# Kernel optimization log

Measured on AMD Instinct MI355X. Metric: run time of the kernel, lower is better.

Reference implementation:

```python
import jax, jax.numpy as jnp
import numpy as np
from math import sqrt

T, B, V = 32, 16, 30000
D, DQKV = 300, 150
K, G = 10, 32            # top-K globals, grapharea_size neighbours each
S = 25000                # last_idx_senses (= SC rows)
EPS = 1e-8


def setup_inputs() -> dict:
    key = jax.random.key(0)
    ks = jax.random.split(key, 6)
    return {
        "predictions_globals": jax.random.normal(ks[0], (T, B, V), jnp.float32),
        "location_context": jax.random.normal(ks[1], (T, B, D), jnp.float32),
        "SC": jax.random.normal(ks[2], (S, D), jnp.float32),
        "Wq": jax.random.normal(ks[3], (D, DQKV), jnp.float32) / sqrt(D),
        "Wk": jax.random.normal(ks[4], (D, DQKV), jnp.float32) / sqrt(D),
        "neighbours_table": jax.random.randint(ks[5], (V, G), 0, S, jnp.int64),
    }


def reference(predictions_globals, location_context, SC, Wq, Wk, neighbours_table):
    # 1) per-sample top-K global selection (sort descending, take K indices)
    _, topk_idx = jax.lax.top_k(predictions_globals, K)          # [T,B,K]
    # 2) sense-neighbour lookup: K globals x G neighbours -> N = K*G senses
    neigh = neighbours_table[topk_idx].reshape(T, B, K * G)      # [T,B,N] int
    # 3) gather precomputed sense contexts
    senses_context = SC[neigh]                                   # [T,B,N,D]
    # 4) ComputeLogits: QK attention logits
    q = location_context @ Wq                                    # [T,B,dqkv]
    k = senses_context @ Wk                                      # [T,B,N,dqkv]
    logits = jnp.einsum("tbd,tbnd->tbn", q, k) / sqrt(DQKV)      # [T,B,N]
    # 5) softmax over neighbours, scatter into full sense distribution
    p = jax.nn.softmax(logits, axis=-1)                          # [T,B,N]
    base = jnp.full((T * B, S), EPS, dtype=p.dtype)
    rows = jnp.arange(T * B)[:, None]                            # [TB,1]
    senses_softmax = base.at[rows, neigh.reshape(T * B, -1)].set(p.reshape(T * B, -1))
    # 6) log-probabilities over all senses
    return jnp.log(senses_softmax)                               # [T*B, S]
```

## Files before the change

### kernel.cpp

```cpp
#include <hip/hip_runtime.h>
#include <math.h>

#define T_ 32
#define B_ 16
#define V_ 30000
#define V4 7500
#define D_ 300
#define DQKV_ 150
#define K_ 10
#define G_ 32
#define N_ 320
#define S_ 25000
#define S4 6250
#define SLICE 3125
#define QKP 304
#define NTS 1024
#define NTG 256
#define NTF 384
#define LCAP 4096
#define UTH 0xC0000000u

__device__ __forceinline__ unsigned umap(float f) {
    unsigned b = __float_as_uint(f);
    unsigned mask = (unsigned)(((int)b) >> 31);
    return b ^ (mask | 0x80000000u);
}
__device__ __forceinline__ bool better_u(unsigned au, int ai, unsigned bu, int bi) {
    return (au > bu) || (au == bu && ai < bi);
}

__global__ __launch_bounds__(NTS, 2) void scanqk_kernel(
    const float* __restrict__ pred, const float* __restrict__ lc,
    const float* __restrict__ Wq, const float* __restrict__ Wk,
    float* __restrict__ out, int* __restrict__ wstop, float* __restrict__ qkws)
{
    const int b = blockIdx.x, tid = threadIdx.x;
    const int lane = tid & 63, wave = tid >> 6;
    __shared__ unsigned lu[LCAP];
    __shared__ int      li[LCAP];
    __shared__ int      cnt;
    __shared__ unsigned wcv[16 * K_];
    __shared__ int      wci[16 * K_];
    __shared__ __align__(16) float lcs[D_];
    __shared__ float    qpart[2][DQKV_];

    if (b >= T_ * B_) {
        const int row = b - T_ * B_;
        if (tid < D_ / 4)
            ((float4*)lcs)[tid] = ((const float4*)(lc + (size_t)row * D_))[tid];
        __syncthreads();

        if (tid < 2 * DQKV_) {
            int h = tid / DQKV_;
            int j = tid - h * DQKV_;
            int d0 = h * 150;
            const float* wp = Wq + (size_t)d0 * DQKV_ + j;
            float a0 = 0.f, a1 = 0.f;
            #pragma unroll 5
            for (int dd = 0; dd < 150; dd += 2) {
                a0 += lcs[d0 + dd]     * wp[(size_t)dd * DQKV_];
                a1 += lcs[d0 + dd + 1] * wp[(size_t)(dd + 1) * DQKV_];
            }
            qpart[h][j] = a0 + a1;
        }
        __syncthreads();

        float qv0 = qpart[0][lane] + qpart[1][lane];
        float qv1 = qpart[0][64 + lane] + qpart[1][64 + lane];
        float qv2 = (lane < 22) ? (qpart[0][128 + lane] + qpart[1][128 + lane]) : 0.f;
        for (int d = wave; d < D_; d += 16) {
            const float* wr = Wk + (size_t)d * DQKV_;
            float w0 = wr[lane];
            float w1 = wr[64 + lane];
            float w2 = (lane < 22) ? wr[128 + lane] : 0.f;
            float p = w0 * qv0 + w1 * qv1 + w2 * qv2;
            #pragma unroll
            for (int off = 32; off; off >>= 1) p += __shfl_xor(p, off, 64);
            if (lane == 0) qkws[(size_t)row * QKP + d] = p;
        }
        return;
    }

    const int row = b;
    if (tid == 0) cnt = 0;
    __syncthreads();

    const float FILL = -18.420680743952367f;
    {
        float4 f4 = make_float4(FILL, FILL, FILL, FILL);
        float4* o4 = (float4*)(out + (size_t)row * S_);
        #pragma unroll
        for (int k = 0; k < 7; ++k) { int i = tid + k * NTS; if (i < S4) o4[i] = f4; }
    }

    {
        const float4* p4 = (const float4*)(pred + (size_t)row * V_);
        #pragma unroll
        for (int k = 0; k < 8; ++k) {
            int i = tid + k * NTS;
            if (i < V4) {
                float4 v = p4[i];
                unsigned u0 = umap(v.x), u1 = umap(v.y), u2 = umap(v.z), u3 = umap(v.w);
                int base = i * 4;
                if (u0 >= UTH) { int p = atomicAdd(&cnt, 1); if (p < LCAP) { lu[p] = u0; li[p] = base; } }
                if (u1 >= UTH) { int p = atomicAdd(&cnt, 1); if (p < LCAP) { lu[p] = u1; li[p] = base + 1; } }
                if (u2 >= UTH) { int p = atomicAdd(&cnt, 1); if (p < LCAP) { lu[p] = u2; li[p] = base + 2; } }
                if (u3 >= UTH) { int p = atomicAdd(&cnt, 1); if (p < LCAP) { lu[p] = u3; li[p] = base + 3; } }
            }
        }
    }
    __syncthreads();
    const int c = cnt;

    if (c >= K_ && c <= LCAP) {
        unsigned cu[4]; int cix[4];
        #pragma unroll
        for (int k = 0; k < 4; ++k) {
            int s = wave * 64 + lane + k * NTS;
            bool ok = s < c;
            cu[k]  = ok ? lu[s] : 0u;
            cix[k] = ok ? li[s] : 0x7fffffff;
        }
        for (int p = 0; p < K_; ++p) {
            unsigned bu = cu[0]; int bi = cix[0];
            #pragma unroll
            for (int k = 1; k < 4; ++k)
                if (better_u(cu[k], cix[k], bu, bi)) { bu = cu[k]; bi = cix[k]; }
            #pragma unroll
            for (int off = 32; off; off >>= 1) {
                unsigned ou = __shfl_xor(bu, off, 64);
                int      oi = __shfl_xor(bi, off, 64);
                if (better_u(ou, oi, bu, bi)) { bu = ou; bi = oi; }
            }
            if (lane == 0) { wcv[wave * K_ + p] = bu; wci[wave * K_ + p] = bi; }
            #pragma unroll
            for (int k = 0; k < 4; ++k)
                if (cix[k] == bi) cu[k] = 0u;
        }
        __syncthreads();

        if (wave == 0) {
            unsigned c0u = wcv[lane],      c1u = wcv[64 + lane];
            int      c0i = wci[lane],      c1i = wci[64 + lane];
            unsigned c2u = (lane < 32) ? wcv[128 + lane] : 0u;
            int      c2i = (lane < 32) ? wci[128 + lane] : 0x7fffffff;
            for (int p = 0; p < K_; ++p) {
                unsigned bu = c0u; int bi = c0i;
                if (better_u(c1u, c1i, bu, bi)) { bu = c1u; bi = c1i; }
                if (better_u(c2u, c2i, bu, bi)) { bu = c2u; bi = c2i; }
                #pragma unroll
                for (int off = 32; off; off >>= 1) {
                    unsigned ou = __shfl_xor(bu, off, 64);
                    int      oi = __shfl_xor(bi, off, 64);
                    if (better_u(ou, oi, bu, bi)) { bu = ou; bi = oi; }
                }
                if (lane == 0) wstop[row * K_ + p] = bi;
                if (c0i == bi) c0u = 0u;
                if (c1i == bi) c1u = 0u;
                if (c2i == bi) c2u = 0u;
            }
        }
    } else {
        if (wave == 0) {
            unsigned tu[K_]; int tix[K_];
            #pragma unroll
            for (int s = 0; s < K_; ++s) { tu[s] = 0; tix[s] = 0x7fffffff; }
            const float* prow = pred + (size_t)row * V_;
            for (int i = lane; i < V_; i += 64) {
                unsigned u = umap(prow[i]);
                if (better_u(u, i, tu[K_-1], tix[K_-1])) {
                    tu[K_-1] = u; tix[K_-1] = i;
                    #pragma unroll
                    for (int s = K_-1; s > 0; --s)
                        if (better_u(tu[s], tix[s], tu[s-1], tix[s-1])) {
                            unsigned a = tu[s]; tu[s] = tu[s-1]; tu[s-1] = a;
                            int b2 = tix[s]; tix[s] = tix[s-1]; tix[s-1] = b2;
                        }
                }
            }
            for (int p = 0; p < K_; ++p) {
                unsigned bu = tu[0]; int bi = tix[0];
                #pragma unroll
                for (int s = 1; s < K_; ++s)
                    if (better_u(tu[s], tix[s], bu, bi)) { bu = tu[s]; bi = tix[s]; }
                #pragma unroll
                for (int off = 32; off; off >>= 1) {
                    unsigned ou = __shfl_xor(bu, off, 64);
                    int      oi = __shfl_xor(bi, off, 64);
                    if (better_u(ou, oi, bu, bi)) { bu = ou; bi = oi; }
                }
                if (lane == 0) wstop[row * K_ + p] = bi;
                #pragma unroll
                for (int s = 0; s < K_; ++s)
                    if (tix[s] == bi) tu[s] = 0;
            }
        }
    }
}

__global__ __launch_bounds__(NTG) void gather_kernel(
    const float* __restrict__ SC, const float* __restrict__ qkws,
    const int* __restrict__ nbt, const int* __restrict__ wstop,
    float* __restrict__ logws)
{
    const int r = blockIdx.x >> 3;
    const int ch = blockIdx.x & 7;
    const int lo = ch * SLICE, hi = lo + SLICE;
    const int tid = threadIdx.x;
    __shared__ int   topg[K_];
    __shared__ int   nid[N_];
    __shared__ __align__(16) float qk[D_];
    __shared__ int   list[N_];
    __shared__ int   lcnt;

    if (tid == 0) lcnt = 0;
    if (tid < K_) topg[tid] = wstop[r * K_ + tid];
    if (tid >= 64 && tid < 64 + D_ / 4)
        ((float4*)qk)[tid - 64] = ((const float4*)(qkws + (size_t)r * QKP))[tid - 64];
    __syncthreads();

    for (int i = tid; i < N_; i += NTG)
        nid[i] = nbt[topg[i >> 5] * G_ + (i & 31)];
    __syncthreads();

    for (int i = tid; i < N_; i += NTG) {
        int sv = nid[i];
        if (sv >= lo && sv < hi) { int p = atomicAdd(&lcnt, 1); list[p] = i; }
    }
    __syncthreads();
    const int c2 = lcnt;

    const float ISC = 0.08164965809277260327f;
    const float4* q4 = (const float4*)qk;
    for (int s = tid; s < 8 * c2; s += NTG) {
        int g = s >> 3, h = s & 7;
        int n = list[g];
        const float4* sc4 = (const float4*)(SC + (size_t)nid[n] * D_);
        int c0 = h * 9;
        float acc = 0.f;
        #pragma unroll
        for (int cc = 0; cc < 9; ++cc) {
            float4 a = sc4[c0 + cc];
            float4 bq = q4[c0 + cc];
            acc += a.x * bq.x + a.y * bq.y + a.z * bq.z + a.w * bq.w;
        }
        if (h < 3) {
            float4 a = sc4[72 + h];
            float4 bq = q4[72 + h];
            acc += a.x * bq.x + a.y * bq.y + a.z * bq.z + a.w * bq.w;
        }
        acc += __shfl_xor(acc, 1, 64);
        acc += __shfl_xor(acc, 2, 64);
        acc += __shfl_xor(acc, 4, 64);
        if (h == 0) logws[(size_t)r * N_ + n] = acc * ISC;
    }
}

__global__ __launch_bounds__(NTF) void finalize_kernel(
    const float* __restrict__ logws, const int* __restrict__ nbt,
    const int* __restrict__ wstop, float* __restrict__ out)
{
    const int row = blockIdx.x, tid = threadIdx.x;
    const int lane = tid & 63, wave = tid >> 6;
    __shared__ int   topg[K_];
    __shared__ float lg[N_];
    __shared__ int   nid[N_];
    __shared__ int   kills[N_];
    __shared__ float redA[6], redB[6];
    float* outrow = out + (size_t)row * S_;

    if (tid < K_) topg[tid] = wstop[row * K_ + tid];
    __syncthreads();
    if (tid < N_) {
        nid[tid] = nbt[topg[tid >> 5] * G_ + (tid & 31)];
        lg[tid]  = logws[(size_t)row * N_ + tid];
        kills[tid] = 0;
    }
    __syncthreads();

    float v = (tid < N_) ? lg[tid] : -INFINITY;
    float m = v;
    #pragma unroll
    for (int off = 32; off; off >>= 1) m = fmaxf(m, __shfl_xor(m, off, 64));
    if (lane == 0) redA[wave] = m;
    __syncthreads();
    m = redA[0];
    #pragma unroll
    for (int w = 1; w < 6; ++w) m = fmaxf(m, redA[w]);

    float ss = (tid < N_) ? expf(v - m) : 0.f;
    #pragma unroll
    for (int off = 32; off; off >>= 1) ss += __shfl_xor(ss, off, 64);
    if (lane == 0) redB[wave] = ss;
    __syncthreads();
    float tot = redB[0];
    #pragma unroll
    for (int w = 1; w < 6; ++w) tot += redB[w];
    float lsum = logf(tot);

    for (int s = tid; s < 4 * N_; s += NTF) {
        int n = s >> 2, cix = s & 3;
        int sidx = nid[n];
        int clo = cix * 80;
        int lo2 = (n + 1 > clo) ? n + 1 : clo;
        int hi2 = clo + 80;
        bool mt = false;
        #pragma unroll 4
        for (int n2 = lo2; n2 < hi2; ++n2) mt |= (nid[n2] == sidx);
        if (mt) kills[n] = 1;
    }
    __syncthreads();

    if (tid < N_ && !kills[tid]) outrow[nid[tid]] = (v - m) - lsum;
}

#define NWS 16
__device__ __forceinline__ bool better(float av, int ai, float bv, int bi) {
    return (av > bv) || (av == bv && ai < bi);
}
__global__ __launch_bounds__(NTS, 4) void selfatt_fused(
    const float* __restrict__ pred, const float* __restrict__ lc,
    const float* __restrict__ SC, const float* __restrict__ Wq,
    const float* __restrict__ Wk, const int* __restrict__ nbt,
    float* __restrict__ out)
{
    const int row = blockIdx.x, tid = threadIdx.x;
    const int lane = tid & 63, wave = tid >> 6;
    __shared__ float wcv[NWS * K_];
    __shared__ int   wci[NWS * K_];
    __shared__ int   topg[K_];
    __shared__ float lcs[D_];
    __shared__ float qs[DQKV_];
    __shared__ __align__(16) float qks[D_];
    __shared__ int   nidx[N_];
    __shared__ float lg[N_];
    __shared__ int   kills[N_];
    __shared__ float redA[NWS], redB[NWS];
    float* outrow = out + (size_t)row * S_;
    const float FILL = -18.420680743952367f;
    {
        float4 f4 = make_float4(FILL, FILL, FILL, FILL);
        float4* o4 = (float4*)outrow;
        #pragma unroll
        for (int k = 0; k < 7; ++k) { int i = tid + k * NTS; if (i < S4) o4[i] = f4; }
    }
    float tv[K_]; int ti[K_];
    #pragma unroll
    for (int s = 0; s < K_; ++s) { tv[s] = -INFINITY; ti[s] = 0x7fffffff; }
    {
        const float4* p4 = (const float4*)(pred + (size_t)row * V_);
        const float4 NEG = make_float4(-INFINITY, -INFINITY, -INFINITY, -INFINITY);
        float4 a[8]; int ib[8];
        #pragma unroll
        for (int u = 0; u < 8; ++u) {
            int i = tid + u * NTS;
            a[u]  = (i < V4) ? p4[i] : NEG;
            ib[u] = (i < V4) ? i * 4 : 0x7ffffff0;
        }
        #pragma unroll
        for (int u = 0; u < 8; ++u) {
            float x = a[u].x, y = a[u].y, z = a[u].z, w = a[u].w;
            float m4 = fmaxf(fmaxf(x, y), fmaxf(z, w));
            if (!(m4 < tv[K_-1])) {
                float vals[4] = {x, y, z, w};
                #pragma unroll
                for (int cc = 0; cc < 4; ++cc) {
                    float val = vals[cc];
                    int   idx = ib[u] + cc;
                    if (better(val, idx, tv[K_-1], ti[K_-1])) {
                        tv[K_-1] = val; ti[K_-1] = idx;
                        #pragma unroll
                        for (int s = K_-1; s > 0; --s) {
                            if (better(tv[s], ti[s], tv[s-1], ti[s-1])) {
                                float fx = tv[s]; tv[s] = tv[s-1]; tv[s-1] = fx;
                                int   iy = ti[s]; ti[s] = ti[s-1]; ti[s-1] = iy;
                            }
                        }
                    }
                }
            }
        }
    }
    for (int p = 0; p < K_; ++p) {
        float bv = tv[0]; int bi = ti[0];
        #pragma unroll
        for (int s = 1; s < K_; ++s)
            if (better(tv[s], ti[s], bv, bi)) { bv = tv[s]; bi = ti[s]; }
        #pragma unroll
        for (int off = 32; off; off >>= 1) {
            float ov = __shfl_xor(bv, off, 64);
            int   oi = __shfl_xor(bi, off, 64);
            if (better(ov, oi, bv, bi)) { bv = ov; bi = oi; }
        }
        if (lane == 0) { wcv[wave * K_ + p] = bv; wci[wave * K_ + p] = bi; }
        #pragma unroll
        for (int s = 0; s < K_; ++s)
            if (ti[s] == bi) tv[s] = -INFINITY;
    }
    __syncthreads();
    if (wave == 0) {
        float c0v = wcv[lane],      c1v = wcv[64 + lane];
        int   c0i = wci[lane],      c1i = wci[64 + lane];
        float c2v = (lane < 32) ? wcv[128 + lane] : -INFINITY;
        int   c2i = (lane < 32) ? wci[128 + lane] : 0x7fffffff;
        for (int p = 0; p < K_; ++p) {
            float bv = c0v; int bi = c0i;
            if (better(c1v, c1i, bv, bi)) { bv = c1v; bi = c1i; }
            if (better(c2v, c2i, bv, bi)) { bv = c2v; bi = c2i; }
            #pragma unroll
            for (int off = 32; off; off >>= 1) {
                float ov = __shfl_xor(bv, off, 64);
                int   oi = __shfl_xor(bi, off, 64);
                if (better(ov, oi, bv, bi)) { bv = ov; bi = oi; }
            }
            if (lane == 0) topg[p] = bi;
            if (c0i == bi) c0v = -INFINITY;
            if (c1i == bi) c1v = -INFINITY;
            if (c2i == bi) c2v = -INFINITY;
        }
    }
    __syncthreads();
    if (tid < N_) { int g = topg[tid >> 5]; nidx[tid] = nbt[g * G_ + (tid & 31)]; }
    else if (tid < 2 * N_) kills[tid - N_] = 0;
    else if (tid >= 640 && tid < 640 + D_) lcs[tid - 640] = lc[(size_t)row * D_ + (tid - 640)];
    __syncthreads();
    if (tid < 600) {
        int j = tid >> 2, h = tid & 3;
        int d0 = h * 75;
        const float* wp = Wq + (size_t)d0 * DQKV_ + j;
        float acc = 0.f;
        #pragma unroll 5
        for (int dd = 0; dd < 75; ++dd) acc += lcs[d0 + dd] * wp[(size_t)dd * DQKV_];
        acc += __shfl_xor(acc, 1, 64);
        acc += __shfl_xor(acc, 2, 64);
        if (h == 0) qs[j] = acc;
    } else {
        int t0 = tid - 600;
        for (int s = t0; s < 4 * N_; s += 424) {
            int n = s >> 2, cc = s & 3;
            int sidx = nidx[n];
            int clo = cc * 80;
            int lo = (n + 1 > clo) ? n + 1 : clo;
            int hi = clo + 80;
            bool mt = false;
            #pragma unroll 4
            for (int n2 = lo; n2 < hi; ++n2) mt |= (nidx[n2] == sidx);
            if (mt) kills[n] = 1;
        }
    }
    __syncthreads();
    if (tid < 600) {
        int d = tid >> 1, h = tid & 1;
        int j0 = h * 75;
        const float* wrow = Wk + (size_t)d * DQKV_ + j0;
        float acc = 0.f;
        #pragma unroll 5
        for (int jj = 0; jj < 75; ++jj) acc += wrow[jj] * qs[j0 + jj];
        acc += __shfl_xor(acc, 1, 64);
        if (h == 0) qks[d] = acc;
    }
    __syncthreads();
    const float ISC = 0.08164965809277260327f;
    const float4* q4 = (const float4*)qks;
    for (int s = tid; s < 8 * N_; s += NTS) {
        int n = s >> 3, h = s & 7;
        const float4* sc4 = (const float4*)(SC + (size_t)nidx[n] * D_);
        int c0 = h * 9;
        float acc = 0.f;
        #pragma unroll
        for (int cc = 0; cc < 9; ++cc) {
            float4 a = sc4[c0 + cc];
            float4 b = q4[c0 + cc];
            acc += a.x * b.x + a.y * b.y + a.z * b.z + a.w * b.w;
        }
        if (h < 3) {
            float4 a = sc4[72 + h];
            float4 b = q4[72 + h];
            acc += a.x * b.x + a.y * b.y + a.z * b.z + a.w * b.w;
        }
        acc += __shfl_xor(acc, 1, 64);
        acc += __shfl_xor(acc, 2, 64);
        acc += __shfl_xor(acc, 4, 64);
        if (h == 0) lg[n] = acc * ISC;
    }
    __syncthreads();
    float v = (tid < N_) ? lg[tid] : -INFINITY;
    float m = v;
    #pragma unroll
    for (int off = 32; off; off >>= 1) m = fmaxf(m, __shfl_xor(m, off, 64));
    if (lane == 0) redA[wave] = m;
    __syncthreads();
    m = redA[0];
    #pragma unroll
    for (int w = 1; w < NWS; ++w) m = fmaxf(m, redA[w]);
    float e = (tid < N_) ? expf(v - m) : 0.f;
    float ss = e;
    #pragma unroll
    for (int off = 32; off; off >>= 1) ss += __shfl_xor(ss, off, 64);
    if (lane == 0) redB[wave] = ss;
    __syncthreads();
    float tot = redB[0];
    #pragma unroll
    for (int w = 1; w < NWS; ++w) tot += redB[w];
    float lsum = logf(tot);
    if (tid < N_ && !kills[tid]) outrow[nidx[tid]] = (v - m) - lsum;
}

extern "C" void kernel_launch(void* const* d_in, const int* in_sizes, int n_in,
                              void* d_out, int out_size, void* d_ws, size_t ws_size,
                              hipStream_t stream) {
    const float* pred = (const float*)d_in[0];
    const float* lc   = (const float*)d_in[1];
    const float* SC   = (const float*)d_in[2];
    const float* Wq   = (const float*)d_in[3];
    const float* Wk   = (const float*)d_in[4];
    const int*   nbt  = (const int*)d_in[5];
    float* out = (float*)d_out;

    const int nrows = T_ * B_;
    const size_t nQK = (size_t)nrows * QKP;
    const size_t nLG = (size_t)nrows * N_;
    const size_t nTP = (size_t)nrows * K_;
    const size_t need = (nQK + nLG) * sizeof(float) + nTP * sizeof(int);

    if (ws_size >= need) {
        float* qkws  = (float*)d_ws;
        float* logws = qkws + nQK;
        int*   wstop = (int*)(logws + nLG);
        scanqk_kernel<<<dim3(nrows * 2), dim3(NTS), 0, stream>>>(
            pred, lc, Wq, Wk, out, wstop, qkws);
        gather_kernel<<<dim3(nrows * 8), dim3(NTG), 0, stream>>>(
            SC, qkws, nbt, wstop, logws);
        finalize_kernel<<<dim3(nrows), dim3(NTF), 0, stream>>>(
            logws, nbt, wstop, out);
    } else {
        selfatt_fused<<<dim3(T_ * B_), dim3(NTS), 0, stream>>>(
            pred, lc, SC, Wq, Wk, nbt, out);
    }
}
```

Before: 101.7 us.

## Fold QK projection into scan blocks and use nontemporal fill stores

Merges the separate q/Wk projection blocks into the top-k scan blocks, so the grid drops from 2x rows to rows. The q projection now runs on idle waves 1-5 while wave 0 does the final top-K merge, and the Wk projection then runs after a shared barrier. The output fill now uses nontemporal vector stores to avoid polluting the cache. The trade-off is that each scan block now does the projection work serially after the top-k, which lengthens each block while cutting the block count.

New measurement: 111.2 us. +9.3%, slower.

```diff
diff --git a/kernel.cpp b/kernel.cpp
--- a/kernel.cpp
+++ b/kernel.cpp
@@ -20,6 +20,8 @@
 #define LCAP 4096
 #define UTH 0xC0000000u
 
+typedef float f32x4 __attribute__((ext_vector_type(4)));
+
 __device__ __forceinline__ unsigned umap(float f) {
     unsigned b = __float_as_uint(f);
     unsigned mask = (unsigned)(((int)b) >> 31);
@@ -34,7 +36,7 @@
     const float* __restrict__ Wq, const float* __restrict__ Wk,
     float* __restrict__ out, int* __restrict__ wstop, float* __restrict__ qkws)
 {
-    const int b = blockIdx.x, tid = threadIdx.x;
+    const int row = blockIdx.x, tid = threadIdx.x;
     const int lane = tid & 63, wave = tid >> 6;
     __shared__ unsigned lu[LCAP];
     __shared__ int      li[LCAP];
@@ -44,53 +46,20 @@
     __shared__ __align__(16) float lcs[D_];
     __shared__ float    qpart[2][DQKV_];
 
-    if (b >= T_ * B_) {
-        const int row = b - T_ * B_;
-        if (tid < D_ / 4)
-            ((float4*)lcs)[tid] = ((const float4*)(lc + (size_t)row * D_))[tid];
-        __syncthreads();
-
-        if (tid < 2 * DQKV_) {
-            int h = tid / DQKV_;
-            int j = tid - h * DQKV_;
-            int d0 = h * 150;
-            const float* wp = Wq + (size_t)d0 * DQKV_ + j;
-            float a0 = 0.f, a1 = 0.f;
-            #pragma unroll 5
-            for (int dd = 0; dd < 150; dd += 2) {
-                a0 += lcs[d0 + dd]     * wp[(size_t)dd * DQKV_];
-                a1 += lcs[d0 + dd + 1] * wp[(size_t)(dd + 1) * DQKV_];
-            }
-            qpart[h][j] = a0 + a1;
-        }
-        __syncthreads();
-
-        float qv0 = qpart[0][lane] + qpart[1][lane];
-        float qv1 = qpart[0][64 + lane] + qpart[1][64 + lane];
-        float qv2 = (lane < 22) ? (qpart[0][128 + lane] + qpart[1][128 + lane]) : 0.f;
-        for (int d = wave; d < D_; d += 16) {
-            const float* wr = Wk + (size_t)d * DQKV_;
-            float w0 = wr[lane];
-            float w1 = wr[64 + lane];
-            float w2 = (lane < 22) ? wr[128 + lane] : 0.f;
-            float p = w0 * qv0 + w1 * qv1 + w2 * qv2;
-            #pragma unroll
-            for (int off = 32; off; off >>= 1) p += __shfl_xor(p, off, 64);
-            if (lane == 0) qkws[(size_t)row * QKP + d] = p;
-        }
-        return;
-    }
-
-    const int row = b;
     if (tid == 0) cnt = 0;
+    if (tid < D_ / 4)
+        ((float4*)lcs)[tid] = ((const float4*)(lc + (size_t)row * D_))[tid];
     __syncthreads();
 
     const float FILL = -18.420680743952367f;
     {
-        float4 f4 = make_float4(FILL, FILL, FILL, FILL);
-        float4* o4 = (float4*)(out + (size_t)row * S_);
-        #pragma unroll
-        for (int k = 0; k < 7; ++k) { int i = tid + k * NTS; if (i < S4) o4[i] = f4; }
+        f32x4 f4 = { FILL, FILL, FILL, FILL };
+        f32x4* o4 = (f32x4*)(out + (size_t)row * S_);
+        #pragma unroll
+        for (int k = 0; k < 7; ++k) {
+            int i = tid + k * NTS;
+            if (i < S4) __builtin_nontemporal_store(f4, o4 + i);
+        }
     }
 
     {
@@ -111,8 +80,9 @@
     }
     __syncthreads();
     const int c = cnt;
-
-    if (c >= K_ && c <= LCAP) {
+    const bool mainpath = (c >= K_ && c <= LCAP);
+
+    if (mainpath) {
         unsigned cu[4]; int cix[4];
         #pragma unroll
         for (int k = 0; k < 4; ++k) {
@@ -137,9 +107,11 @@
             for (int k = 0; k < 4; ++k)
                 if (cix[k] == bi) cu[k] = 0u;
         }
-        __syncthreads();
-
-        if (wave == 0) {
+    }
+    __syncthreads();
+
+    if (wave == 0) {
+        if (mainpath) {
             unsigned c0u = wcv[lane],      c1u = wcv[64 + lane];
             int      c0i = wci[lane],      c1i = wci[64 + lane];
             unsigned c2u = (lane < 32) ? wcv[128 + lane] : 0u;
@@ -159,9 +131,7 @@
                 if (c1i == bi) c1u = 0u;
                 if (c2i == bi) c2u = 0u;
             }
-        }
-    } else {
-        if (wave == 0) {
+        } else {
             unsigned tu[K_]; int tix[K_];
             #pragma unroll
             for (int s = 0; s < K_; ++s) { tu[s] = 0; tix[s] = 0x7fffffff; }
@@ -194,6 +164,36 @@
                 for (int s = 0; s < K_; ++s)
                     if (tix[s] == bi) tu[s] = 0;
             }
+        }
+    } else if (tid >= 64 && tid < 64 + 2 * DQKV_) {
+        int t = tid - 64;
+        int h = t / DQKV_;
+        int j = t - h * DQKV_;
+        int d0 = h * 150;
+        const float* wp = Wq + (size_t)d0 * DQKV_ + j;
+        float a0 = 0.f, a1 = 0.f;
+        #pragma unroll 5
+        for (int dd = 0; dd < 150; dd += 2) {
+            a0 += lcs[d0 + dd]     * wp[(size_t)dd * DQKV_];
+            a1 += lcs[d0 + dd + 1] * wp[(size_t)(dd + 1) * DQKV_];
+        }
+        qpart[h][j] = a0 + a1;
+    }
+    __syncthreads();
+
+    {
+        float qv0 = qpart[0][lane] + qpart[1][lane];
+        float qv1 = qpart[0][64 + lane] + qpart[1][64 + lane];
+        float qv2 = (lane < 22) ? (qpart[0][128 + lane] + qpart[1][128 + lane]) : 0.f;
+        for (int d = wave; d < D_; d += 16) {
+            const float* wr = Wk + (size_t)d * DQKV_;
+            float w0 = wr[lane];
+            float w1 = wr[64 + lane];
+            float w2 = (lane < 22) ? wr[128 + lane] : 0.f;
+            float p = w0 * qv0 + w1 * qv1 + w2 * qv2;
+            #pragma unroll
+            for (int off = 32; off; off >>= 1) p += __shfl_xor(p, off, 64);
+            if (lane == 0) qkws[(size_t)row * QKP + d] = p;
         }
     }
 }
@@ -527,7 +527,7 @@
         float* qkws  = (float*)d_ws;
         float* logws = qkws + nQK;
         int*   wstop = (int*)(logws + nLG);
-        scanqk_kernel<<<dim3(nrows * 2), dim3(NTS), 0, stream>>>(
+        scanqk_kernel<<<dim3(nrows), dim3(NTS), 0, stream>>>(
             pred, lc, Wq, Wk, out, wstop, qkws);
         gather_kernel<<<dim3(nrows * 8), dim3(NTG), 0, stream>>>(
             SC, qkws, nbt, wstop, logws);
```

## Split q/k precompute into a batched kernel and use wave-aggregated candidate atomics

Applied to the files above, without the earlier changes.

The q·Wk precompute moves out of the scan kernel's extra 512 blocks into its own 32-block kernel. Each block handles 16 rows, so the Wq and Wk loads are reused across several rows. The top-K candidate scan now issues all its loads up front and replaces per-element LDS atomics with a ballot, popcount and one atomic per wave. This trades one extra kernel launch and a lower-parallelism q/k kernel (only 32 blocks) for less weight traffic and less atomic contention.

After: 192.8 us. +89.6%, slower.

```diff
diff --git a/kernel.cpp b/kernel.cpp
--- a/kernel.cpp
+++ b/kernel.cpp
@@ -17,6 +17,8 @@
 #define NTS 1024
 #define NTG 256
 #define NTF 384
+#define NQB 32
+#define QROWS 16
 #define LCAP 4096
 #define UTH 0xC0000000u
 
@@ -29,59 +31,82 @@
     return (au > bu) || (au == bu && ai < bi);
 }
 
-__global__ __launch_bounds__(NTS, 2) void scanqk_kernel(
-    const float* __restrict__ pred, const float* __restrict__ lc,
-    const float* __restrict__ Wq, const float* __restrict__ Wk,
-    float* __restrict__ out, int* __restrict__ wstop, float* __restrict__ qkws)
+__global__ __launch_bounds__(512) void qkprep_kernel(
+    const float* __restrict__ lc, const float* __restrict__ Wq,
+    const float* __restrict__ Wk, float* __restrict__ qkws)
 {
-    const int b = blockIdx.x, tid = threadIdx.x;
+    __shared__ __align__(16) float lcs[QROWS][304];
+    __shared__ float qlds[QROWS][152];
+    const int r0  = blockIdx.x * QROWS;
+    const int tid = threadIdx.x;
+    const int lane = tid & 63, wv = tid >> 6;
+
+    {
+        const float4* src = (const float4*)(lc + (size_t)r0 * D_);
+        for (int i = tid; i < QROWS * 75; i += 512) {
+            int r = i / 75, c = i - r * 75;
+            *(float4*)&lcs[r][c * 4] = src[i];
+        }
+    }
+    __syncthreads();
+
+    if (tid < 2 * DQKV_) {
+        int j = tid % DQKV_, h = tid / DQKV_;
+        float acc[8];
+        #pragma unroll
+        for (int rr = 0; rr < 8; ++rr) acc[rr] = 0.f;
+        for (int d = 0; d < D_; ++d) {
+            float w = Wq[(size_t)d * DQKV_ + j];
+            #pragma unroll
+            for (int rr = 0; rr < 8; ++rr) acc[rr] += lcs[h * 8 + rr][d] * w;
+        }
+        #pragma unroll
+        for (int rr = 0; rr < 8; ++rr) qlds[h * 8 + rr][j] = acc[rr];
+    }
+    __syncthreads();
+
+    for (int dd = wv; dd < D_; dd += 8) {
+        const float* wr = Wk + (size_t)dd * DQKV_;
+        float w0 = wr[lane];
+        float w1 = wr[64 + lane];
+        float w2 = (lane < 22) ? wr[128 + lane] : 0.f;
+        #pragma unroll
+        for (int rb = 0; rb < QROWS; rb += 4) {
+            float p[4];
+            #pragma unroll
+            for (int i = 0; i < 4; ++i) {
+                int r = rb + i;
+                float q0 = qlds[r][lane];
+                float q1 = qlds[r][64 + lane];
+                float q2 = (lane < 22) ? qlds[r][128 + lane] : 0.f;
+                p[i] = w0 * q0 + w1 * q1 + w2 * q2;
+            }
+            #pragma unroll
+            for (int off = 32; off; off >>= 1) {
+                #pragma unroll
+                for (int i = 0; i < 4; ++i) p[i] += __shfl_xor(p[i], off, 64);
+            }
+            if (lane == 0) {
+                #pragma unroll
+                for (int i = 0; i < 4; ++i)
+                    qkws[(size_t)(r0 + rb + i) * QKP + dd] = p[i];
+            }
+        }
+    }
+}
+
+__global__ __launch_bounds__(NTS, 2) void scan_kernel(
+    const float* __restrict__ pred, float* __restrict__ out,
+    int* __restrict__ wstop)
+{
+    const int row = blockIdx.x, tid = threadIdx.x;
     const int lane = tid & 63, wave = tid >> 6;
     __shared__ unsigned lu[LCAP];
     __shared__ int      li[LCAP];
     __shared__ int      cnt;
     __shared__ unsigned wcv[16 * K_];
     __shared__ int      wci[16 * K_];
-    __shared__ __align__(16) float lcs[D_];
-    __shared__ float    qpart[2][DQKV_];
-
-    if (b >= T_ * B_) {
-        const int row = b - T_ * B_;
-        if (tid < D_ / 4)
-            ((float4*)lcs)[tid] = ((const float4*)(lc + (size_t)row * D_))[tid];
-        __syncthreads();
-
-        if (tid < 2 * DQKV_) {
-            int h = tid / DQKV_;
-            int j = tid - h * DQKV_;
-            int d0 = h * 150;
-            const float* wp = Wq + (size_t)d0 * DQKV_ + j;
-            float a0 = 0.f, a1 = 0.f;
-            #pragma unroll 5
-            for (int dd = 0; dd < 150; dd += 2) {
-                a0 += lcs[d0 + dd]     * wp[(size_t)dd * DQKV_];
-                a1 += lcs[d0 + dd + 1] * wp[(size_t)(dd + 1) * DQKV_];
-            }
-            qpart[h][j] = a0 + a1;
-        }
-        __syncthreads();
-
-        float qv0 = qpart[0][lane] + qpart[1][lane];
-        float qv1 = qpart[0][64 + lane] + qpart[1][64 + lane];
-        float qv2 = (lane < 22) ? (qpart[0][128 + lane] + qpart[1][128 + lane]) : 0.f;
-        for (int d = wave; d < D_; d += 16) {
-            const float* wr = Wk + (size_t)d * DQKV_;
-            float w0 = wr[lane];
-            float w1 = wr[64 + lane];
-            float w2 = (lane < 22) ? wr[128 + lane] : 0.f;
-            float p = w0 * qv0 + w1 * qv1 + w2 * qv2;
-            #pragma unroll
-            for (int off = 32; off; off >>= 1) p += __shfl_xor(p, off, 64);
-            if (lane == 0) qkws[(size_t)row * QKP + d] = p;
-        }
-        return;
-    }
-
-    const int row = b;
+
     if (tid == 0) cnt = 0;
     __syncthreads();
 
@@ -95,24 +120,42 @@
 
     {
         const float4* p4 = (const float4*)(pred + (size_t)row * V_);
-        #pragma unroll
-        for (int k = 0; k < 8; ++k) {
-            int i = tid + k * NTS;
-            if (i < V4) {
-                float4 v = p4[i];
-                unsigned u0 = umap(v.x), u1 = umap(v.y), u2 = umap(v.z), u3 = umap(v.w);
-                int base = i * 4;
-                if (u0 >= UTH) { int p = atomicAdd(&cnt, 1); if (p < LCAP) { lu[p] = u0; li[p] = base; } }
-                if (u1 >= UTH) { int p = atomicAdd(&cnt, 1); if (p < LCAP) { lu[p] = u1; li[p] = base + 1; } }
-                if (u2 >= UTH) { int p = atomicAdd(&cnt, 1); if (p < LCAP) { lu[p] = u2; li[p] = base + 2; } }
-                if (u3 >= UTH) { int p = atomicAdd(&cnt, 1); if (p < LCAP) { lu[p] = u3; li[p] = base + 3; } }
+        const float4 NEG = make_float4(-INFINITY, -INFINITY, -INFINITY, -INFINITY);
+        float4 a[8]; int ib[8]; bool okf[8];
+        #pragma unroll
+        for (int u = 0; u < 8; ++u) {
+            int i = tid + u * NTS;
+            okf[u] = i < V4;
+            a[u]  = okf[u] ? p4[i] : NEG;
+            ib[u] = i * 4;
+        }
+        const unsigned long long lmask = (lane == 63) ? 0x7fffffffffffffffull
+                                                      : ((1ull << lane) - 1ull);
+        #pragma unroll
+        for (int u = 0; u < 8; ++u) {
+            float vals[4] = {a[u].x, a[u].y, a[u].z, a[u].w};
+            #pragma unroll
+            for (int c = 0; c < 4; ++c) {
+                unsigned uu = umap(vals[c]);
+                bool has = okf[u] && (uu >= UTH);
+                unsigned long long mask = __ballot(has);
+                if (mask) {
+                    int bs = 0;
+                    if (lane == 0) bs = atomicAdd(&cnt, (int)__popcll(mask));
+                    bs = __shfl(bs, 0, 64);
+                    if (has) {
+                        int p = bs + (int)__popcll(mask & lmask);
+                        if (p < LCAP) { lu[p] = uu; li[p] = ib[u] + c; }
+                    }
+                }
             }
         }
     }
     __syncthreads();
     const int c = cnt;
-
-    if (c >= K_ && c <= LCAP) {
+    const bool mainpath = (c >= K_ && c <= LCAP);
+
+    if (mainpath) {
         unsigned cu[4]; int cix[4];
         #pragma unroll
         for (int k = 0; k < 4; ++k) {
@@ -527,8 +570,8 @@
         float* qkws  = (float*)d_ws;
         float* logws = qkws + nQK;
         int*   wstop = (int*)(logws + nLG);
-        scanqk_kernel<<<dim3(nrows * 2), dim3(NTS), 0, stream>>>(
-            pred, lc, Wq, Wk, out, wstop, qkws);
+        qkprep_kernel<<<dim3(NQB), dim3(512), 0, stream>>>(lc, Wq, Wk, qkws);
+        scan_kernel<<<dim3(nrows), dim3(NTS), 0, stream>>>(pred, out, wstop);
         gather_kernel<<<dim3(nrows * 8), dim3(NTG), 0, stream>>>(
             SC, qkws, nbt, wstop, logws);
         finalize_kernel<<<dim3(nrows), dim3(NTF), 0, stream>>>(
```

## Split top-K scan into two half-row blocks with wave-aggregated atomics

Applied to the files above, without the earlier changes.

The first stage now uses 256-thread blocks, two per row. Each block scans half of the predictions, fills half of the output row and writes its local top-10 candidates to workspace. The gather and finalize kernels then merge the 20 candidates with a wave shuffle reduction. Candidate appends now use one ballot-based atomic per wave instead of one per element. The goal is more blocks and occupancy and less shared-atomic contention, at the cost of a redundant merge in every gather block.

New measurement: 116.2 us. 1.14x slower.

```diff
diff --git a/kernel.cpp b/kernel.cpp
--- a/kernel.cpp
+++ b/kernel.cpp
@@ -5,6 +5,7 @@
 #define B_ 16
 #define V_ 30000
 #define V4 7500
+#define H4P 3750
 #define D_ 300
 #define DQKV_ 150
 #define K_ 10
@@ -12,12 +13,15 @@
 #define N_ 320
 #define S_ 25000
 #define S4 6250
+#define F4H 3125
 #define SLICE 3125
 #define QKP 304
-#define NTS 1024
+#define NT1 256
+#define NSCAN 1024
+#define NQK 512
 #define NTG 256
 #define NTF 384
-#define LCAP 4096
+#define LCAP2 2048
 #define UTH 0xC0000000u
 
 __device__ __forceinline__ unsigned umap(float f) {
@@ -29,30 +33,26 @@
     return (au > bu) || (au == bu && ai < bi);
 }
 
-__global__ __launch_bounds__(NTS, 2) void scanqk_kernel(
+__global__ __launch_bounds__(NT1, 6) void stage1_kernel(
     const float* __restrict__ pred, const float* __restrict__ lc,
     const float* __restrict__ Wq, const float* __restrict__ Wk,
-    float* __restrict__ out, int* __restrict__ wstop, float* __restrict__ qkws)
+    float* __restrict__ out, unsigned* __restrict__ wsu, int* __restrict__ wsi,
+    float* __restrict__ qkws)
 {
     const int b = blockIdx.x, tid = threadIdx.x;
     const int lane = tid & 63, wave = tid >> 6;
-    __shared__ unsigned lu[LCAP];
-    __shared__ int      li[LCAP];
-    __shared__ int      cnt;
-    __shared__ unsigned wcv[16 * K_];
-    __shared__ int      wci[16 * K_];
-    __shared__ __align__(16) float lcs[D_];
-    __shared__ float    qpart[2][DQKV_];
-
-    if (b >= T_ * B_) {
-        const int row = b - T_ * B_;
+
+    if (b >= NSCAN) {
+        const int row = b - NSCAN;
+        __shared__ __align__(16) float lcs[D_];
+        __shared__ float qpart[2][DQKV_];
         if (tid < D_ / 4)
             ((float4*)lcs)[tid] = ((const float4*)(lc + (size_t)row * D_))[tid];
         __syncthreads();
 
-        if (tid < 2 * DQKV_) {
-            int h = tid / DQKV_;
-            int j = tid - h * DQKV_;
+        for (int t = tid; t < 2 * DQKV_; t += NT1) {
+            int h = t / DQKV_;
+            int j = t - h * DQKV_;
             int d0 = h * 150;
             const float* wp = Wq + (size_t)d0 * DQKV_ + j;
             float a0 = 0.f, a1 = 0.f;
@@ -68,7 +68,7 @@
         float qv0 = qpart[0][lane] + qpart[1][lane];
         float qv1 = qpart[0][64 + lane] + qpart[1][64 + lane];
         float qv2 = (lane < 22) ? (qpart[0][128 + lane] + qpart[1][128 + lane]) : 0.f;
-        for (int d = wave; d < D_; d += 16) {
+        for (int d = wave; d < D_; d += 4) {
             const float* wr = Wk + (size_t)d * DQKV_;
             float w0 = wr[lane];
             float w1 = wr[64 + lane];
@@ -81,42 +81,68 @@
         return;
     }
 
-    const int row = b;
+    const int row  = b >> 1;
+    const int half = b & 1;
+    __shared__ unsigned lu[LCAP2];
+    __shared__ int      li[LCAP2];
+    __shared__ int      cnt;
+    __shared__ unsigned wcv[4 * K_];
+    __shared__ int      wci[4 * K_];
+
     if (tid == 0) cnt = 0;
     __syncthreads();
 
     const float FILL = -18.420680743952367f;
     {
         float4 f4 = make_float4(FILL, FILL, FILL, FILL);
-        float4* o4 = (float4*)(out + (size_t)row * S_);
-        #pragma unroll
-        for (int k = 0; k < 7; ++k) { int i = tid + k * NTS; if (i < S4) o4[i] = f4; }
+        float4* o4 = (float4*)(out + (size_t)row * S_) + half * F4H;
+        for (int i = tid; i < F4H; i += NT1) o4[i] = f4;
     }
 
     {
-        const float4* p4 = (const float4*)(pred + (size_t)row * V_);
+        const float4* p4 = (const float4*)(pred + (size_t)row * V_) + half * H4P;
+        const int gbase = half * (H4P * 4);
+        const unsigned long long lmask = (lane == 63) ? 0x7fffffffffffffffull
+                                                      : ((1ull << lane) - 1ull);
+        for (int t = 0; t < 5; ++t) {
+            float4 a[3]; int ib[3]; bool okf[3];
+            #pragma unroll
+            for (int u = 0; u < 3; ++u) {
+                int i = tid + (t * 3 + u) * NT1;
+                okf[u] = i < H4P;
+                a[u]  = okf[u] ? p4[i]
+                               : make_float4(-INFINITY, -INFINITY, -INFINITY, -INFINITY);
+                ib[u] = gbase + i * 4;
+            }
+            #pragma unroll
+            for (int u = 0; u < 3; ++u) {
+                float vals[4] = {a[u].x, a[u].y, a[u].z, a[u].w};
+                #pragma unroll
+                for (int c = 0; c < 4; ++c) {
+                    unsigned uu = umap(vals[c]);
+                    bool has = okf[u] && (uu >= UTH);
+                    unsigned long long mask = __ballot(has);
+                    if (mask) {
+                        int bs = 0;
+                        if (lane == 0) bs = atomicAdd(&cnt, (int)__popcll(mask));
+                        bs = __shfl(bs, 0, 64);
+                        if (has) {
+                            int p = bs + (int)__popcll(mask & lmask);
+                            if (p < LCAP2) { lu[p] = uu; li[p] = ib[u] + c; }
+                        }
+                    }
+                }
+            }
+        }
+    }
+    __syncthreads();
+    const int c = cnt;
+
+    if (c >= K_ && c <= LCAP2) {
+        unsigned cu[8]; int cix[8];
         #pragma unroll
         for (int k = 0; k < 8; ++k) {
-            int i = tid + k * NTS;
-            if (i < V4) {
-                float4 v = p4[i];
-                unsigned u0 = umap(v.x), u1 = umap(v.y), u2 = umap(v.z), u3 = umap(v.w);
-                int base = i * 4;
-                if (u0 >= UTH) { int p = atomicAdd(&cnt, 1); if (p < LCAP) { lu[p] = u0; li[p] = base; } }
-                if (u1 >= UTH) { int p = atomicAdd(&cnt, 1); if (p < LCAP) { lu[p] = u1; li[p] = base + 1; } }
-                if (u2 >= UTH) { int p = atomicAdd(&cnt, 1); if (p < LCAP) { lu[p] = u2; li[p] = base + 2; } }
-                if (u3 >= UTH) { int p = atomicAdd(&cnt, 1); if (p < LCAP) { lu[p] = u3; li[p] = base + 3; } }
-            }
-        }
-    }
-    __syncthreads();
-    const int c = cnt;
-
-    if (c >= K_ && c <= LCAP) {
-        unsigned cu[4]; int cix[4];
-        #pragma unroll
-        for (int k = 0; k < 4; ++k) {
-            int s = wave * 64 + lane + k * NTS;
+            int s = wave * 64 + lane + k * NT1;
             bool ok = s < c;
             cu[k]  = ok ? lu[s] : 0u;
             cix[k] = ok ? li[s] : 0x7fffffff;
@@ -124,7 +150,7 @@
         for (int p = 0; p < K_; ++p) {
             unsigned bu = cu[0]; int bi = cix[0];
             #pragma unroll
-            for (int k = 1; k < 4; ++k)
+            for (int k = 1; k < 8; ++k)
                 if (better_u(cu[k], cix[k], bu, bi)) { bu = cu[k]; bi = cix[k]; }
             #pragma unroll
             for (int off = 32; off; off >>= 1) {
@@ -134,30 +160,27 @@
             }
             if (lane == 0) { wcv[wave * K_ + p] = bu; wci[wave * K_ + p] = bi; }
             #pragma unroll
-            for (int k = 0; k < 4; ++k)
+            for (int k = 0; k < 8; ++k)
                 if (cix[k] == bi) cu[k] = 0u;
         }
         __syncthreads();
 
         if (wave == 0) {
-            unsigned c0u = wcv[lane],      c1u = wcv[64 + lane];
-            int      c0i = wci[lane],      c1i = wci[64 + lane];
-            unsigned c2u = (lane < 32) ? wcv[128 + lane] : 0u;
-            int      c2i = (lane < 32) ? wci[128 + lane] : 0x7fffffff;
+            unsigned cv = (lane < 40) ? wcv[lane] : 0u;
+            int      ci = (lane < 40) ? wci[lane] : 0x7fffffff;
             for (int p = 0; p < K_; ++p) {
-                unsigned bu = c0u; int bi = c0i;
-                if (better_u(c1u, c1i, bu, bi)) { bu = c1u; bi = c1i; }
-                if (better_u(c2u, c2i, bu, bi)) { bu = c2u; bi = c2i; }
+                unsigned bu = cv; int bi = ci;
                 #pragma unroll
                 for (int off = 32; off; off >>= 1) {
                     unsigned ou = __shfl_xor(bu, off, 64);
                     int      oi = __shfl_xor(bi, off, 64);
                     if (better_u(ou, oi, bu, bi)) { bu = ou; bi = oi; }
                 }
-                if (lane == 0) wstop[row * K_ + p] = bi;
-                if (c0i == bi) c0u = 0u;
-                if (c1i == bi) c1u = 0u;
-                if (c2i == bi) c2u = 0u;
+                if (lane == 0) {
+                    wsu[(row * 2 + half) * K_ + p] = bu;
+                    wsi[(row * 2 + half) * K_ + p] = bi;
+                }
+                if (ci == bi) cv = 0u;
             }
         }
     } else {
@@ -165,11 +188,13 @@
             unsigned tu[K_]; int tix[K_];
             #pragma unroll
             for (int s = 0; s < K_; ++s) { tu[s] = 0; tix[s] = 0x7fffffff; }
-            const float* prow = pred + (size_t)row * V_;
-            for (int i = lane; i < V_; i += 64) {
+            const float* prow = pred + (size_t)row * V_ + half * (H4P * 4);
+            const int gbase = half * (H4P * 4);
+            for (int i = lane; i < H4P * 4; i += 64) {
                 unsigned u = umap(prow[i]);
-                if (better_u(u, i, tu[K_-1], tix[K_-1])) {
-                    tu[K_-1] = u; tix[K_-1] = i;
+                int gi = gbase + i;
+                if (better_u(u, gi, tu[K_-1], tix[K_-1])) {
+                    tu[K_-1] = u; tix[K_-1] = gi;
                     #pragma unroll
                     for (int s = K_-1; s > 0; --s)
                         if (better_u(tu[s], tix[s], tu[s-1], tix[s-1])) {
@@ -189,7 +214,10 @@
                     int      oi = __shfl_xor(bi, off, 64);
                     if (better_u(ou, oi, bu, bi)) { bu = ou; bi = oi; }
                 }
-                if (lane == 0) wstop[row * K_ + p] = bi;
+                if (lane == 0) {
+                    wsu[(row * 2 + half) * K_ + p] = bu;
+                    wsi[(row * 2 + half) * K_ + p] = bi;
+                }
                 #pragma unroll
                 for (int s = 0; s < K_; ++s)
                     if (tix[s] == bi) tu[s] = 0;
@@ -198,15 +226,35 @@
     }
 }
 
+__device__ __forceinline__ void merge20(
+    const unsigned* __restrict__ wsu, const int* __restrict__ wsi,
+    int row, int lane, int* topg)
+{
+    unsigned cv = (lane < 2 * K_) ? wsu[row * 2 * K_ + lane] : 0u;
+    int      ci = (lane < 2 * K_) ? wsi[row * 2 * K_ + lane] : 0x7fffffff;
+    for (int p = 0; p < K_; ++p) {
+        unsigned bu = cv; int bi = ci;
+        #pragma unroll
+        for (int off = 32; off; off >>= 1) {
+            unsigned ou = __shfl_xor(bu, off, 64);
+            int      oi = __shfl_xor(bi, off, 64);
+            if (better_u(ou, oi, bu, bi)) { bu = ou; bi = oi; }
+        }
+        if (lane == 0) topg[p] = bi;
+        if (ci == bi) cv = 0u;
+    }
+}
+
 __global__ __launch_bounds__(NTG) void gather_kernel(
     const float* __restrict__ SC, const float* __restrict__ qkws,
-    const int* __restrict__ nbt, const int* __restrict__ wstop,
-    float* __restrict__ logws)
+    const int* __restrict__ nbt, const unsigned* __restrict__ wsu,
+    const int* __restrict__ wsi, float* __restrict__ logws)
 {
     const int r = blockIdx.x >> 3;
     const int ch = blockIdx.x & 7;
     const int lo = ch * SLICE, hi = lo + SLICE;
     const int tid = threadIdx.x;
+    const int lane = tid & 63, wave = tid >> 6;
     __shared__ int   topg[K_];
     __shared__ int   nid[N_];
     __shared__ __align__(16) float qk[D_];
@@ -214,7 +262,7 @@
     __shared__ int   lcnt;
 
     if (tid == 0) lcnt = 0;
-    if (tid < K_) topg[tid] = wstop[r * K_ + tid];
+    if (wave == 0) merge20(wsu, wsi, r, lane, topg);
     if (tid >= 64 && tid < 64 + D_ / 4)
         ((float4*)qk)[tid - 64] = ((const float4*)(qkws + (size_t)r * QKP))[tid - 64];
     __syncthreads();
@@ -258,7 +306,8 @@
 
 __global__ __launch_bounds__(NTF) void finalize_kernel(
     const float* __restrict__ logws, const int* __restrict__ nbt,
-    const int* __restrict__ wstop, float* __restrict__ out)
+    const unsigned* __restrict__ wsu, const int* __restrict__ wsi,
+    float* __restrict__ out)
 {
     const int row = blockIdx.x, tid = threadIdx.x;
     const int lane = tid & 63, wave = tid >> 6;
@@ -269,7 +318,7 @@
     __shared__ float redA[6], redB[6];
     float* outrow = out + (size_t)row * S_;
 
-    if (tid < K_) topg[tid] = wstop[row * K_ + tid];
+    if (wave == 0) merge20(wsu, wsi, row, lane, topg);
     __syncthreads();
     if (tid < N_) {
         nid[tid] = nbt[topg[tid >> 5] * G_ + (tid & 31)];
@@ -315,6 +364,7 @@
 }
 
 #define NWS 16
+#define NTS 1024
 __device__ __forceinline__ bool better(float av, int ai, float bv, int bi) {
     return (av > bv) || (av == bv && ai < bi);
 }
@@ -520,21 +570,22 @@
     const int nrows = T_ * B_;
     const size_t nQK = (size_t)nrows * QKP;
     const size_t nLG = (size_t)nrows * N_;
-    const size_t nTP = (size_t)nrows * K_;
-    const size_t need = (nQK + nLG) * sizeof(float) + nTP * sizeof(int);
+    const size_t nCD = (size_t)nrows * 2 * K_;
+    const size_t need = (nQK + nLG) * sizeof(float) + nCD * (sizeof(int) + 4);
 
     if (ws_size >= need) {
-        float* qkws  = (float*)d_ws;
-        float* logws = qkws + nQK;
-        int*   wstop = (int*)(logws + nLG);
-        scanqk_kernel<<<dim3(nrows * 2), dim3(NTS), 0, stream>>>(
-            pred, lc, Wq, Wk, out, wstop, qkws);
+        float*    qkws  = (float*)d_ws;
+        float*    logws = qkws + nQK;
+        unsigned* wsu   = (unsigned*)(logws + nLG);
+        int*      wsi   = (int*)(wsu + nCD);
+        stage1_kernel<<<dim3(NSCAN + NQK), dim3(NT1), 0, stream>>>(
+            pred, lc, Wq, Wk, out, wsu, wsi, qkws);
         gather_kernel<<<dim3(nrows * 8), dim3(NTG), 0, stream>>>(
-            SC, qkws, nbt, wstop, logws);
+            SC, qkws, nbt, wsu, wsi, logws);
         finalize_kernel<<<dim3(nrows), dim3(NTF), 0, stream>>>(
-            logws, nbt, wstop, out);
+            logws, nbt, wsu, wsi, out);
     } else {
-        selfatt_fused<<<dim3(T_ * B_), dim3(NTS), 0, stream>>>(
+        selfatt_fused<<<dim3(nrows), dim3(NTS), 0, stream>>>(
             pred, lc, SC, Wq, Wk, nbt, out);
     }
 }
```
